# Optimization experiments

Measured on AMD Instinct MI355X. Metric: run time of the kernel, lower is better.

The kernel has to match this reference:

```python
import jax, jax.numpy as jnp
import numpy as np
from jax.scipy.special import logsumexp

B, D, A = 64, 128, 128


def setup_inputs() -> dict:
    key = jax.random.key(0)
    k1, k2, k3, k4 = jax.random.split(key, 4)
    x = jax.random.randint(k1, (B, D), 0, 2).astype(jnp.float32)  # binary observations
    u_log_p_a1 = jax.random.normal(k2, (1, 1, 1, A), dtype=jnp.float32)
    u_log_transition = jax.random.normal(k3, (D - 1, A, A), dtype=jnp.float32)
    log_p_xi_g_ai = jax.random.normal(k4, (1, D, 1, A), dtype=jnp.float32)
    return {
        "x": x,
        "u_log_p_a1": u_log_p_a1,
        "u_log_transition": u_log_transition,
        "log_p_xi_g_ai": log_p_xi_g_ai,
    }


def reference(x, u_log_p_a1, u_log_transition, log_p_xi_g_ai):
    b, d = x.shape
    a = u_log_p_a1.shape[-1]
    # _normalize_logits == log_softmax along last dim
    log_p_a1 = jax.nn.log_softmax(u_log_p_a1, axis=-1)          # [1,1,1,A]
    log_T = jax.nn.log_softmax(u_log_transition, axis=-1)        # [D-1,A,A]
    # Bernoulli(logits=l).log_prob(v) = v*l - softplus(l)
    l = log_p_xi_g_ai                                            # [1,D,1,A]
    log_px_vec = x[:, :, None, None] * l - jax.nn.softplus(l)    # [B,D,1,A]
    # per-step reduction matrices
    red = log_px_vec[:, 1:] + log_T                              # [B,D-1,A,A]
    # initial matrix: row-repeated initial vector
    init = jnp.broadcast_to(log_px_vec[:, 0] + log_p_a1[0], (b, a, a))  # [B,A,A]
    mats = jnp.transpose(red, (1, 0, 2, 3))                      # [D-1,B,A,A]

    def step(M, T):
        # log-space matmul: new[b,i,j] = logsumexp_k M[b,i,k] + T[b,k,j]
        new = logsumexp(M[:, :, :, None] + T[:, None, :, :], axis=2)
        return new, None

    final, _ = jax.lax.scan(step, init, mats)                    # [B,A,A]
    log_px = logsumexp(final, axis=-1)                           # [B,A] (rows identical)
    return (log_px, log_p_a1)
```

## Files before the change

### kernel.cpp

```cpp
#include <hip/hip_runtime.h>


#define B_ 64
#define D_ 128
#define A_ 128
#define T_ 127

#define E16_UINTS (T_ * 8192)
#define BC_OFF E16_UINTS
#define BC_SZ (B_ * T_ * A_)
#define LP_OFF (BC_OFF + BC_SZ)

typedef _Float16 h2 __attribute__((ext_vector_type(2)));

__device__ __forceinline__ float dot2acc(unsigned int e, unsigned int s, float acc) {
    return __builtin_amdgcn_fdot2(__builtin_bit_cast(h2, e),
                                  __builtin_bit_cast(h2, s), acc, false);
}
__device__ __forceinline__ int packrtz(float a, float b) {
    auto p = __builtin_amdgcn_cvt_pkrtz(a, b);
    return __builtin_bit_cast(int, p);
}

template <int CTRL>
__device__ __forceinline__ float dpp_mov_self(float x) {
    return __int_as_float(__builtin_amdgcn_update_dpp(
        __float_as_int(x), __float_as_int(x), CTRL, 0xF, 0xF, false));
}
template <int CTRL>
__device__ __forceinline__ float dpp_mov_zero(float x) {
    return __int_as_float(__builtin_amdgcn_update_dpp(
        0, __float_as_int(x), CTRL, 0xF, 0xF, true));
}
__device__ __forceinline__ float wave_max_partial(float x) {
    x = fmaxf(x, dpp_mov_self<0x111>(x));
    x = fmaxf(x, dpp_mov_self<0x112>(x));
    x = fmaxf(x, dpp_mov_self<0x114>(x));
    x = fmaxf(x, dpp_mov_self<0x118>(x));
    x = fmaxf(x, dpp_mov_self<0x142>(x));
    x = fmaxf(x, dpp_mov_self<0x143>(x));
    return x;
}
__device__ __forceinline__ float wave_max_bcast(float x) {
    return __int_as_float(__builtin_amdgcn_readlane(
        __float_as_int(wave_max_partial(x)), 63));
}
__device__ __forceinline__ float wave_sum_bcast(float x) {
    x += dpp_mov_zero<0x111>(x);
    x += dpp_mov_zero<0x112>(x);
    x += dpp_mov_zero<0x114>(x);
    x += dpp_mov_zero<0x118>(x);
    x += dpp_mov_zero<0x142>(x);
    x += dpp_mov_zero<0x143>(x);
    return __int_as_float(__builtin_amdgcn_readlane(__float_as_int(x), 63));
}

__global__ __launch_bounds__(256) void prep(const float* __restrict__ uT,
                                            const float* __restrict__ u1,
                                            const float* __restrict__ x,
                                            const float* __restrict__ lg,
                                            float* __restrict__ ws,
                                            float* __restrict__ out) {
    __shared__ float ul[128 * 128];
    const int t = blockIdx.x, tid = threadIdx.x;
    const float* u = uT + (size_t)t * A_ * A_;

    for (int i = tid; i < 4096; i += 256) {
        float4 v4 = ((const float4*)u)[i];
        *(float4*)&ul[(i >> 5) * 128 + (i & 31) * 4] = v4;
    }
    __syncthreads();

    if (tid < 128) {
        const int r = tid;
        float mx = -1e30f;
        for (int it = 0; it < 128; it++) mx = fmaxf(mx, ul[r * 128 + ((it + r) & 127)]);
        float s = 0.f;
        for (int it = 0; it < 128; it++) s += __expf(ul[r * 128 + ((it + r) & 127)] - mx);
        float Z = mx + __logf(s);
        for (int it = 0; it < 128; it++) ul[r * 128 + ((it + r) & 127)] -= Z;
    }
    __syncthreads();

    unsigned int* Et = (unsigned int*)ws + (size_t)t * 8192;
    for (int it = 0; it < 32; it++) {
        int a = it * 256 + tid;
        int c = a & 3, j = (a >> 2) & 127, q = a >> 9;
        int i = 4 * q + c;
        float e0 = __expf(ul[(2 * i) * 128 + j]);
        float e1 = __expf(ul[(2 * i + 1) * 128 + j]);
        Et[a] = (unsigned int)packrtz(e0, e1);
    }

    {
        int j = tid & 127, hb = tid >> 7;
        float lv = lg[(t + 1) * A_ + j];
        float sp = (lv > 0.f) ? (lv + log1pf(__expf(-lv))) : log1pf(__expf(lv));
        float g0 = -sp, g1 = lv - sp;
        float* BC = ws + BC_OFF;
        for (int b = hb * 32; b < hb * 32 + 32; b++) {
            float xv = x[b * D_ + t + 1];
            BC[((size_t)b * T_ + t) * A_ + j] = (xv != 0.f) ? g1 : g0;
        }
    }

    if (t == 0 && tid < 64) {
        int lane = tid;
        float a = u1[lane], c = u1[lane + 64];
        float mx = wave_max_bcast(fmaxf(a, c));
        float s = wave_sum_bcast(__expf(a - mx) + __expf(c - mx));
        float lse = mx + __logf(s);
        ws[LP_OFF + lane] = a - lse;
        ws[LP_OFF + lane + 64] = c - lse;
        out[B_ * A_ + lane] = a - lse;
        out[B_ * A_ + lane + 64] = c - lse;
    }
}

#define BARRIER() asm volatile("s_waitcnt lgkmcnt(0)\n\ts_barrier" ::: "memory")

#define STEP(T, EC, EP, BCC, BCP, DOPF)                                       \
    {                                                                         \
        const int p = (T) & 1, np = p ^ 1;                                    \
        if (DOPF) {                                    \
            const uint4* pfp = (const uint4*)(Eb + (size_t)((T) + 1) * 32768);\
            _Pragma("unroll") for (int q = 0; q < 16; q++) EP[q] = pfp[q*128];\
            BCP = BCg[((T) + 1) * A_];                                        \
            __builtin_amdgcn_sched_barrier(0);                                \
        }                                                                     \
        float2 vm2 = *(const float2*)&vml[p][0];                              \
        float Mcur = fmaxf(vm2.x, vm2.y);                                     \
        const uint4* ewp = (const uint4*)&ewl[p][0];                          \
        float a0 = 0, a1 = 0, a2 = 0, a3 = 0;                                 \
        _Pragma("unroll") for (int q = 0; q < 16; q++) {                      \
            uint4 e = ewp[q];                                                 \
            a0 = dot2acc(EC[q].x, e.x, a0);                                   \
            a1 = dot2acc(EC[q].y, e.y, a1);                                   \
            a2 = dot2acc(EC[q].z, e.z, a2);                                   \
            a3 = dot2acc(EC[q].w, e.w, a3);                                   \
        }                                                                     \
        float S = (a0 + a1) + (a2 + a3);                                      \
        float vnew = __logf(S) + Mp + BCC;                                    \
        ewl[np][j] = (_Float16)__expf(vnew - Mcur);   \
        float wm = wave_max_partial(vnew);             \
        if (lane == 63) vml[np][w] = wm;                                      \
        v = vnew;                                                             \
        Mp = Mcur;                                                            \
        BARRIER();                                                            \
    }

__global__ __launch_bounds__(128) void fwd(const float* __restrict__ x,
                                           const float* __restrict__ lg,
                                           const float* __restrict__ ws,
                                           float* __restrict__ out) {
    __shared__ __align__(16) _Float16 ewl[2][A_];
    __shared__ float vml[2][2];
    __shared__ float sums[2];
    const int b = blockIdx.x, tid = threadIdx.x;
    const int w = tid >> 6, lane = tid & 63;
    const int j = 64 * w + lane;

    const char* Eb = (const char*)ws + j * 16;
    const float* BCg = ws + BC_OFF + (size_t)b * T_ * A_ + j;
    const float* LP = ws + LP_OFF;

    float ll = lg[j];
    float sp = (ll > 0.f) ? (ll + log1pf(__expf(-ll))) : log1pf(__expf(ll));
    float xv0 = x[b * D_];
    float v = LP[j] + ((xv0 != 0.f) ? (ll - sp) : (-sp));
    float wm0 = wave_max_bcast(v);
    if (lane == 0) vml[0][w] = wm0;
    BARRIER();
    float Mp = fmaxf(vml[0][0], vml[0][1]);
    ewl[0][j] = (_Float16)__expf(v - Mp);

    uint4 E0[16], E1[16];
    float bc0, bc1;
    {
        const uint4* p0 = (const uint4*)(Eb);
#pragma unroll
        for (int q = 0; q < 16; q++) E0[q] = p0[q * 128];
        bc0 = BCg[0];
        __builtin_amdgcn_sched_barrier(0);
    }
    bc1 = 0.f;
    BARRIER();

    for (int t = 0; t < 126; t += 2) {
        STEP(t + 0, E0, E1, bc0, bc1, 1)
        STEP(t + 1, E1, E0, bc1, bc0, 1)
    }
    STEP(126, E0, E1, bc0, bc1, 0)

    float Mf = fmaxf(vml[1][0], vml[1][1]);
    float sw = wave_sum_bcast(__expf(v - Mf));
    if (lane == 0) sums[w] = sw;
    BARRIER();
    float L = Mf + __logf(sums[0] + sums[1]);
    out[b * A_ + j] = L;
}

extern "C" void kernel_launch(void* const* d_in, const int* in_sizes, int n_in,
                              void* d_out, int out_size, void* d_ws, size_t ws_size,
                              hipStream_t stream) {
    const float* x = (const float*)d_in[0];
    const float* u1 = (const float*)d_in[1];
    const float* uT = (const float*)d_in[2];
    const float* lg = (const float*)d_in[3];
    float* ws = (float*)d_ws;
    float* out = (float*)d_out;

    prep<<<dim3(T_), dim3(256), 0, stream>>>(uT, u1, x, lg, ws, out);
    fwd<<<dim3(B_), dim3(128), 0, stream>>>(x, lg, ws, out);
}
```

Measured before the change: 177.1 us.

## Store transition exponentials as fp8 and stream them via global-to-LDS triple buffering

Transition probability matrices are now precomputed as scaled fp8 (x256, with the scale compensated in the emission bias) instead of fp16. The forward kernel uses 256 threads that split the k-reduction in halves across lanes, and it triple-buffers the per-step matrix through LDS with async global_load_lds instead of register prefetch. The goal is to halve memory traffic per step and hide load latency behind compute. Using fp8 adds significant quantization error to the log-likelihood recurrence, and the extra per-step __syncthreads plus unpack conversions add overhead.

```diff
diff --git a/kernel.cpp b/kernel.cpp
--- a/kernel.cpp
+++ b/kernel.cpp
@@ -5,22 +5,65 @@
 #define D_ 128
 #define A_ 128
 #define T_ 127
-
-#define E16_UINTS (T_ * 8192)
-#define BC_OFF E16_UINTS
+#define LN256 5.545177444479562f
+
+#define E8_UINTS (T_ * 4096)
+#define BC_OFF E8_UINTS
 #define BC_SZ (B_ * T_ * A_)
 #define LP_OFF (BC_OFF + BC_SZ)
 
-typedef _Float16 h2 __attribute__((ext_vector_type(2)));
-
-__device__ __forceinline__ float dot2acc(unsigned int e, unsigned int s, float acc) {
-    return __builtin_amdgcn_fdot2(__builtin_bit_cast(h2, e),
-                                  __builtin_bit_cast(h2, s), acc, false);
-}
-__device__ __forceinline__ int packrtz(float a, float b) {
-    auto p = __builtin_amdgcn_cvt_pkrtz(a, b);
-    return __builtin_bit_cast(int, p);
-}
+#define AS1C(p) ((const __attribute__((address_space(1))) void*)(p))
+#define AS3P(p) ((__attribute__((address_space(3))) void*)(p))
+
+typedef float f2v __attribute__((ext_vector_type(2)));
+
+#if __has_builtin(__builtin_amdgcn_cvt_pk_f32_fp8)
+template <int WORD>
+__device__ __forceinline__ f2v unpk(unsigned int u) {
+    return __builtin_amdgcn_cvt_pk_f32_fp8((int)u, WORD);
+}
+#else
+__device__ __forceinline__ float fp8b_to_f32(unsigned int b) {
+    unsigned int e = (b >> 3) & 15, m = b & 7;
+    if (e) return __uint_as_float(((e + 120) << 23) | (m << 20));
+    return (float)m * 0x1p-9f;
+}
+template <int WORD>
+__device__ __forceinline__ f2v unpk(unsigned int u) {
+    unsigned int b0 = (u >> (WORD ? 16 : 0)) & 255;
+    unsigned int b1 = (u >> (WORD ? 24 : 8)) & 255;
+    f2v r; r.x = fp8b_to_f32(b0); r.y = fp8b_to_f32(b1);
+    return r;
+}
+#endif
+
+#if __has_builtin(__builtin_amdgcn_cvt_pk_fp8_f32)
+__device__ __forceinline__ unsigned int pk4_fp8(float a, float b, float c, float d) {
+    int v = __builtin_amdgcn_cvt_pk_fp8_f32(a, b, 0, false);
+    v = __builtin_amdgcn_cvt_pk_fp8_f32(c, d, v, true);
+    return (unsigned int)v;
+}
+#else
+__device__ __forceinline__ unsigned int f32_to_fp8b(float f) {
+    if (f < 0.015625f) {
+        int m = (int)rintf(f * 512.f);
+        return (unsigned int)m;
+    }
+    unsigned int fb = __float_as_uint(f);
+    int ex = (int)((fb >> 23) & 255) - 127;
+    unsigned int mant = (fb >> 20) & 7;
+    unsigned int rem = fb & 0xFFFFFu;
+    if (rem > 0x80000u || (rem == 0x80000u && (mant & 1))) mant++;
+    int e8 = ex + 7;
+    if (mant == 8) { mant = 0; e8++; }
+    if (e8 > 15) return 0x7Eu;
+    return ((unsigned int)e8 << 3) | mant;
+}
+__device__ __forceinline__ unsigned int pk4_fp8(float a, float b, float c, float d) {
+    return f32_to_fp8b(a) | (f32_to_fp8b(b) << 8) |
+           (f32_to_fp8b(c) << 16) | (f32_to_fp8b(d) << 24);
+}
+#endif
 
 template <int CTRL>
 __device__ __forceinline__ float dpp_mov_self(float x) {
@@ -82,21 +125,26 @@
     }
     __syncthreads();
 
-    unsigned int* Et = (unsigned int*)ws + (size_t)t * 8192;
-    for (int it = 0; it < 32; it++) {
-        int a = it * 256 + tid;
-        int c = a & 3, j = (a >> 2) & 127, q = a >> 9;
-        int i = 4 * q + c;
-        float e0 = __expf(ul[(2 * i) * 128 + j]);
-        float e1 = __expf(ul[(2 * i + 1) * 128 + j]);
-        Et[a] = (unsigned int)packrtz(e0, e1);
+    unsigned int* Et = (unsigned int*)ws + (size_t)t * 4096;
+    for (int it = 0; it < 16; it++) {
+        int m = it * 256 + tid;
+        int g = m >> 7;
+        int c = g >> 3, h = (g >> 2) & 1, w = g & 3;
+        int jl = (m >> 2) & 31;
+        int k0 = 64 * h + 16 * c + 4 * (m & 3);
+        int j = 32 * w + jl;
+        float f0 = 256.f * __expf(ul[(k0 + 0) * 128 + j]);
+        float f1 = 256.f * __expf(ul[(k0 + 1) * 128 + j]);
+        float f2 = 256.f * __expf(ul[(k0 + 2) * 128 + j]);
+        float f3 = 256.f * __expf(ul[(k0 + 3) * 128 + j]);
+        Et[m] = pk4_fp8(f0, f1, f2, f3);
     }
 
     {
         int j = tid & 127, hb = tid >> 7;
         float lv = lg[(t + 1) * A_ + j];
         float sp = (lv > 0.f) ? (lv + log1pf(__expf(-lv))) : log1pf(__expf(lv));
-        float g0 = -sp, g1 = lv - sp;
+        float g0 = -sp - LN256, g1 = lv - sp - LN256;
         float* BC = ws + BC_OFF;
         for (int b = hb * 32; b < hb * 32 + 32; b++) {
             float xv = x[b * D_ + t + 1];
@@ -117,87 +165,116 @@
     }
 }
 
-#define BARRIER() asm volatile("s_waitcnt lgkmcnt(0)\n\ts_barrier" ::: "memory")
-
-#define STEP(T, EC, EP, BCC, BCP, DOPF)                                       \
+#define STEP(T, BUFC, BUFN, P, DOISSUE)                                       \
     {                                                                         \
-        const int p = (T) & 1, np = p ^ 1;                                    \
-        if (DOPF) {                                    \
-            const uint4* pfp = (const uint4*)(Eb + (size_t)((T) + 1) * 32768);\
-            _Pragma("unroll") for (int q = 0; q < 16; q++) EP[q] = pfp[q*128];\
-            BCP = BCg[((T) + 1) * A_];                                        \
-            __builtin_amdgcn_sched_barrier(0);                                \
+        __syncthreads();                                                      \
+        uint4 ec0 = *(const uint4*)&Ebuf[BUFC][((0 + h) * 4 + w) * 512 + jl * 16]; \
+        uint4 ec1 = *(const uint4*)&Ebuf[BUFC][((2 + h) * 4 + w) * 512 + jl * 16]; \
+        uint4 ec2 = *(const uint4*)&Ebuf[BUFC][((4 + h) * 4 + w) * 512 + jl * 16]; \
+        uint4 ec3 = *(const uint4*)&Ebuf[BUFC][((6 + h) * 4 + w) * 512 + jl * 16]; \
+        if (DOISSUE) {                                                        \
+            _Pragma("unroll") for (int i = 0; i < 4; i++)                     \
+                __builtin_amdgcn_global_load_lds(                             \
+                    AS1C(Eg + ((size_t)(T) + 2) * 16384 + (w * 4 + i) * 1024  \
+                         + lane * 16),                                        \
+                    AS3P(&Ebuf[BUFN][(w * 4 + i) * 1024]), 16, 0, 0);         \
         }                                                                     \
-        float2 vm2 = *(const float2*)&vml[p][0];                              \
-        float Mcur = fmaxf(vm2.x, vm2.y);                                     \
-        const uint4* ewp = (const uint4*)&ewl[p][0];                          \
+        float4 vm = *(const float4*)&vml[P][0];                               \
+        float Mv = fmaxf(fmaxf(vm.x, vm.y), fmaxf(vm.z, vm.w));               \
         float a0 = 0, a1 = 0, a2 = 0, a3 = 0;                                 \
-        _Pragma("unroll") for (int q = 0; q < 16; q++) {                      \
-            uint4 e = ewp[q];                                                 \
-            a0 = dot2acc(EC[q].x, e.x, a0);                                   \
-            a1 = dot2acc(EC[q].y, e.y, a1);                                   \
-            a2 = dot2acc(EC[q].z, e.z, a2);                                   \
-            a3 = dot2acc(EC[q].w, e.w, a3);                                   \
+        _Pragma("unroll") for (int c = 0; c < 4; c++) {                       \
+            uint4 ec = (c == 0) ? ec0 : (c == 1) ? ec1 : (c == 2) ? ec2 : ec3;\
+            const float4* ewp = (const float4*)&ewf[P][64 * h + 16 * c];      \
+            float4 w0 = ewp[0], w1 = ewp[1], w2 = ewp[2], w3 = ewp[3];        \
+            f2v p0 = unpk<0>(ec.x), p1 = unpk<1>(ec.x);                       \
+            a0 += p0.x * w0.x; a1 += p0.y * w0.y;                             \
+            a2 += p1.x * w0.z; a3 += p1.y * w0.w;                             \
+            f2v p2 = unpk<0>(ec.y), p3 = unpk<1>(ec.y);                       \
+            a0 += p2.x * w1.x; a1 += p2.y * w1.y;                             \
+            a2 += p3.x * w1.z; a3 += p3.y * w1.w;                             \
+            f2v p4 = unpk<0>(ec.z), p5 = unpk<1>(ec.z);                       \
+            a0 += p4.x * w2.x; a1 += p4.y * w2.y;                             \
+            a2 += p5.x * w2.z; a3 += p5.y * w2.w;                             \
+            f2v p6 = unpk<0>(ec.w), p7 = unpk<1>(ec.w);                       \
+            a0 += p6.x * w3.x; a1 += p6.y * w3.y;                             \
+            a2 += p7.x * w3.z; a3 += p7.y * w3.w;                             \
         }                                                                     \
         float S = (a0 + a1) + (a2 + a3);                                      \
-        float vnew = __logf(S) + Mp + BCC;                                    \
-        ewl[np][j] = (_Float16)__expf(vnew - Mcur);   \
-        float wm = wave_max_partial(vnew);             \
-        if (lane == 63) vml[np][w] = wm;                                      \
+        S += __shfl_xor(S, 32, 64);                                           \
+        float vnew = __logf(S) + Mn + bcc;                                    \
+        if (h == 0) ewf[P ^ 1][j] = __expf(vnew - Mv);                        \
+        float wmx = wave_max_partial(vnew);                                   \
+        if (lane == 63) vml[P ^ 1][w] = wmx;                                  \
         v = vnew;                                                             \
-        Mp = Mcur;                                                            \
-        BARRIER();                                                            \
-    }
-
-__global__ __launch_bounds__(128) void fwd(const float* __restrict__ x,
-                                           const float* __restrict__ lg,
-                                           const float* __restrict__ ws,
-                                           float* __restrict__ out) {
-    __shared__ __align__(16) _Float16 ewl[2][A_];
-    __shared__ float vml[2][2];
-    __shared__ float sums[2];
+        Mn = Mv;                                                              \
+        bcc = bcn;                                                            \
+        if (DOISSUE) bcn = BCg[((T) + 2) * A_];                               \
+    }
+
+__global__ __launch_bounds__(256, 1) void fwd(const float* __restrict__ x,
+                                              const float* __restrict__ lg,
+                                              const float* __restrict__ ws,
+                                              float* __restrict__ out) {
+    __shared__ __align__(16) char Ebuf[3][16384];
+    __shared__ __align__(16) float ewf[2][A_];
+    __shared__ __align__(16) float vml[2][4];
+    __shared__ float sums[4];
     const int b = blockIdx.x, tid = threadIdx.x;
     const int w = tid >> 6, lane = tid & 63;
-    const int j = 64 * w + lane;
-
-    const char* Eb = (const char*)ws + j * 16;
+    const int h = lane >> 5, jl = lane & 31;
+    const int j = 32 * w + jl;
+
+    const char* Eg = (const char*)ws;
     const float* BCg = ws + BC_OFF + (size_t)b * T_ * A_ + j;
     const float* LP = ws + LP_OFF;
+
+#pragma unroll
+    for (int i = 0; i < 4; i++) {
+        __builtin_amdgcn_global_load_lds(
+            AS1C(Eg + (w * 4 + i) * 1024 + lane * 16),
+            AS3P(&Ebuf[0][(w * 4 + i) * 1024]), 16, 0, 0);
+        __builtin_amdgcn_global_load_lds(
+            AS1C(Eg + 16384 + (w * 4 + i) * 1024 + lane * 16),
+            AS3P(&Ebuf[1][(w * 4 + i) * 1024]), 16, 0, 0);
+    }
+    float bcc = BCg[0];
+    float bcn = BCg[A_];
 
     float ll = lg[j];
     float sp = (ll > 0.f) ? (ll + log1pf(__expf(-ll))) : log1pf(__expf(ll));
     float xv0 = x[b * D_];
     float v = LP[j] + ((xv0 != 0.f) ? (ll - sp) : (-sp));
-    float wm0 = wave_max_bcast(v);
-    if (lane == 0) vml[0][w] = wm0;
-    BARRIER();
-    float Mp = fmaxf(vml[0][0], vml[0][1]);
-    ewl[0][j] = (_Float16)__expf(v - Mp);
-
-    uint4 E0[16], E1[16];
-    float bc0, bc1;
-    {
-        const uint4* p0 = (const uint4*)(Eb);
-#pragma unroll
-        for (int q = 0; q < 16; q++) E0[q] = p0[q * 128];
-        bc0 = BCg[0];
-        __builtin_amdgcn_sched_barrier(0);
-    }
-    bc1 = 0.f;
-    BARRIER();
-
-    for (int t = 0; t < 126; t += 2) {
-        STEP(t + 0, E0, E1, bc0, bc1, 1)
-        STEP(t + 1, E1, E0, bc1, bc0, 1)
-    }
-    STEP(126, E0, E1, bc0, bc1, 0)
-
-    float Mf = fmaxf(vml[1][0], vml[1][1]);
-    float sw = wave_sum_bcast(__expf(v - Mf));
+    float wm0 = wave_max_partial(v);
+    if (lane == 63) vml[0][w] = wm0;
+    __syncthreads();
+    float4 vm0 = *(const float4*)&vml[0][0];
+    float Mn = fmaxf(fmaxf(vm0.x, vm0.y), fmaxf(vm0.z, vm0.w));
+    if (h == 0) ewf[0][j] = __expf(v - Mn);
+
+    for (int t = 0; t < 120; t += 6) {
+        STEP(t + 0, 0, 2, 0, 1)
+        STEP(t + 1, 1, 0, 1, 1)
+        STEP(t + 2, 2, 1, 0, 1)
+        STEP(t + 3, 0, 2, 1, 1)
+        STEP(t + 4, 1, 0, 0, 1)
+        STEP(t + 5, 2, 1, 1, 1)
+    }
+    STEP(120, 0, 2, 0, 1)
+    STEP(121, 1, 0, 1, 1)
+    STEP(122, 2, 1, 0, 1)
+    STEP(123, 0, 2, 1, 1)
+    STEP(124, 1, 0, 0, 1)
+    STEP(125, 2, 1, 1, 0)
+    STEP(126, 0, 2, 0, 0)
+
+    __syncthreads();
+    float4 vmf = *(const float4*)&vml[1][0];
+    float Mf = fmaxf(fmaxf(vmf.x, vmf.y), fmaxf(vmf.z, vmf.w));
+    float sw = wave_sum_bcast(__expf(v - Mf)) * 0.5f;
     if (lane == 0) sums[w] = sw;
-    BARRIER();
-    float L = Mf + __logf(sums[0] + sums[1]);
-    out[b * A_ + j] = L;
+    __syncthreads();
+    float L = Mf + __logf((sums[0] + sums[1]) + (sums[2] + sums[3]));
+    if (tid < A_) out[b * A_ + tid] = L;
 }
 
 extern "C" void kernel_launch(void* const* d_in, const int* in_sizes, int n_in,
@@ -211,5 +288,5 @@
     float* out = (float*)d_out;
 
     prep<<<dim3(T_), dim3(256), 0, stream>>>(uT, u1, x, lg, ws, out);
-    fwd<<<dim3(B_), dim3(128), 0, stream>>>(x, lg, ws, out);
-}
+    fwd<<<dim3(B_), dim3(256), 0, stream>>>(x, lg, ws, out);
+}
```

After: 212.9 us. 20.3% more time.

## Move forward recursion to linear-domain scaling and split the K reduction across half-waves

Applied to the files above, without the earlier changes.

The emission term is now precomputed in exp space, so each step multiplies by it instead of taking a log and exp per element. The running max is handled as a multiplicative rescale whose log is accumulated in beta. The fwd kernel doubles to 256 threads, and each output column's 128-wide dot product is split across two half-waves and combined with a shuffle. Prefetch of the next step's transition tiles uses hand-written global loads with explicit vmcnt waits, and the workspace E layout is permuted to match. This shortens the per-step serial chain of transcendentals and halves the register footprint for E. The cost is an extra shuffle and risk of fp16 range issues in the linear domain.

```diff
diff --git a/kernel.cpp b/kernel.cpp
--- a/kernel.cpp
+++ b/kernel.cpp
@@ -7,19 +7,20 @@
 #define T_ 127
 
 #define E16_UINTS (T_ * 8192)
-#define BC_OFF E16_UINTS
-#define BC_SZ (B_ * T_ * A_)
-#define LP_OFF (BC_OFF + BC_SZ)
+#define G_OFF E16_UINTS
+#define G_SZ (B_ * T_ * A_)
+#define LP_OFF (G_OFF + G_SZ)
 
 typedef _Float16 h2 __attribute__((ext_vector_type(2)));
-
+typedef unsigned int u32x4 __attribute__((ext_vector_type(4)));
+
+__device__ __forceinline__ int packrtz(float a, float b) {
+    auto p = __builtin_amdgcn_cvt_pkrtz(a, b);
+    return __builtin_bit_cast(int, p);
+}
 __device__ __forceinline__ float dot2acc(unsigned int e, unsigned int s, float acc) {
     return __builtin_amdgcn_fdot2(__builtin_bit_cast(h2, e),
                                   __builtin_bit_cast(h2, s), acc, false);
-}
-__device__ __forceinline__ int packrtz(float a, float b) {
-    auto p = __builtin_amdgcn_cvt_pkrtz(a, b);
-    return __builtin_bit_cast(int, p);
 }
 
 template <int CTRL>
@@ -85,8 +86,10 @@
     unsigned int* Et = (unsigned int*)ws + (size_t)t * 8192;
     for (int it = 0; it < 32; it++) {
         int a = it * 256 + tid;
-        int c = a & 3, j = (a >> 2) & 127, q = a >> 9;
-        int i = 4 * q + c;
+        int c = a & 3, jl = (a >> 2) & 31, w = (a >> 7) & 3;
+        int h = (a >> 9) & 1, q = a >> 10;
+        int i = 32 * h + 4 * q + c;
+        int j = 32 * w + jl;
         float e0 = __expf(ul[(2 * i) * 128 + j]);
         float e1 = __expf(ul[(2 * i + 1) * 128 + j]);
         Et[a] = (unsigned int)packrtz(e0, e1);
@@ -96,11 +99,11 @@
         int j = tid & 127, hb = tid >> 7;
         float lv = lg[(t + 1) * A_ + j];
         float sp = (lv > 0.f) ? (lv + log1pf(__expf(-lv))) : log1pf(__expf(lv));
-        float g0 = -sp, g1 = lv - sp;
-        float* BC = ws + BC_OFF;
+        float G0 = __expf(-sp), G1 = __expf(lv - sp);
+        float* G = ws + G_OFF;
         for (int b = hb * 32; b < hb * 32 + 32; b++) {
             float xv = x[b * D_ + t + 1];
-            BC[((size_t)b * T_ + t) * A_ + j] = (xv != 0.f) ? g1 : g0;
+            G[((size_t)b * T_ + t) * A_ + j] = (xv != 0.f) ? G1 : G0;
         }
     }
 
@@ -119,85 +122,114 @@
 
 #define BARRIER() asm volatile("s_waitcnt lgkmcnt(0)\n\ts_barrier" ::: "memory")
 
-#define STEP(T, EC, EP, BCC, BCP, DOPF)                                       \
+#define ISSUE(EN, GN, TT)                                                     \
+    {                                                                         \
+        unsigned long long ab = Ebase + (unsigned long long)(TT) * 32768ull;  \
+        _Pragma("unroll") for (int q = 0; q < 8; q++)                         \
+            asm volatile("global_load_dwordx4 %0, %1, off"                    \
+                         : "=v"(EN[q])                                        \
+                         : "v"(ab + (unsigned long long)(q * 4096)));         \
+        asm volatile("global_load_dword %0, %1, off"                          \
+                     : "=v"(GN)                                               \
+                     : "v"(Gbase + (unsigned long long)(TT) * 512ull));       \
+    }
+
+#define WAITON(EC, GC, CNT)                                                   \
+    asm volatile("s_waitcnt vmcnt(" #CNT ")"                                  \
+                 : "+v"(EC[0]), "+v"(EC[1]), "+v"(EC[2]), "+v"(EC[3]),        \
+                   "+v"(EC[4]), "+v"(EC[5]), "+v"(EC[6]), "+v"(EC[7]),        \
+                   "+v"(GC));
+
+#define BODY(T, EC, GC)                                                       \
     {                                                                         \
         const int p = (T) & 1, np = p ^ 1;                                    \
-        if (DOPF) {                                    \
-            const uint4* pfp = (const uint4*)(Eb + (size_t)((T) + 1) * 32768);\
-            _Pragma("unroll") for (int q = 0; q < 16; q++) EP[q] = pfp[q*128];\
-            BCP = BCg[((T) + 1) * A_];                                        \
-            __builtin_amdgcn_sched_barrier(0);                                \
-        }                                                                     \
-        float2 vm2 = *(const float2*)&vml[p][0];                              \
-        float Mcur = fmaxf(vm2.x, vm2.y);                                     \
-        const uint4* ewp = (const uint4*)&ewl[p][0];                          \
+        float4 vm4 = *(const float4*)&vml[p][0];                              \
+        float maxW = fmaxf(fmaxf(vm4.x, vm4.y), fmaxf(vm4.z, vm4.w));         \
+        float srec = 1.0f / maxW;                                             \
+        beta += __logf(mprev);               \
+        mprev = maxW;                                                         \
+        const uint4* ewp = (const uint4*)&ewl[p][0] + h * 8;                  \
         float a0 = 0, a1 = 0, a2 = 0, a3 = 0;                                 \
-        _Pragma("unroll") for (int q = 0; q < 16; q++) {                      \
-            uint4 e = ewp[q];                                                 \
-            a0 = dot2acc(EC[q].x, e.x, a0);                                   \
-            a1 = dot2acc(EC[q].y, e.y, a1);                                   \
-            a2 = dot2acc(EC[q].z, e.z, a2);                                   \
-            a3 = dot2acc(EC[q].w, e.w, a3);                                   \
+        _Pragma("unroll") for (int q = 0; q < 8; q++) {                       \
+            uint4 ew4 = ewp[q];                                               \
+            a0 = dot2acc(EC[q].x, ew4.x, a0);                                 \
+            a1 = dot2acc(EC[q].y, ew4.y, a1);                                 \
+            a2 = dot2acc(EC[q].z, ew4.z, a2);                                 \
+            a3 = dot2acc(EC[q].w, ew4.w, a3);                                 \
         }                                                                     \
         float S = (a0 + a1) + (a2 + a3);                                      \
-        float vnew = __logf(S) + Mp + BCC;                                    \
-        ewl[np][j] = (_Float16)__expf(vnew - Mcur);   \
-        float wm = wave_max_partial(vnew);             \
-        if (lane == 63) vml[np][w] = wm;                                      \
-        v = vnew;                                                             \
-        Mp = Mcur;                                                            \
+        S += __shfl_xor(S, 32, 64);                                           \
+        float W = S * GC;                                                     \
+        if (h == 0) ewl[np][j] = (_Float16)(W * srec);                        \
+        float wm = wave_max_partial(W);                         \
+        if (lane == 63) vml[np][wv] = wm;                                     \
+        Wlast = W;                                                            \
         BARRIER();                                                            \
     }
 
-__global__ __launch_bounds__(128) void fwd(const float* __restrict__ x,
-                                           const float* __restrict__ lg,
-                                           const float* __restrict__ ws,
-                                           float* __restrict__ out) {
+#define STEPP(T, EC, EN, GC, GN)                                              \
+    {                                                                         \
+        ISSUE(EN, GN, (T) + 1)                                                \
+        WAITON(EC, GC, 9)                                                     \
+        BODY(T, EC, GC)                                                       \
+    }
+#define STEPL(T, EC, GC)                                                      \
+    {                                                                         \
+        WAITON(EC, GC, 0)                                                     \
+        BODY(T, EC, GC)                                                       \
+    }
+
+__global__ __launch_bounds__(256, 1) void fwd(const float* __restrict__ x,
+                                              const float* __restrict__ lg,
+                                              const float* __restrict__ ws,
+                                              float* __restrict__ out) {
     __shared__ __align__(16) _Float16 ewl[2][A_];
-    __shared__ float vml[2][2];
-    __shared__ float sums[2];
+    __shared__ __align__(16) float vml[2][4];
+    __shared__ float sums[4];
     const int b = blockIdx.x, tid = threadIdx.x;
-    const int w = tid >> 6, lane = tid & 63;
-    const int j = 64 * w + lane;
-
-    const char* Eb = (const char*)ws + j * 16;
-    const float* BCg = ws + BC_OFF + (size_t)b * T_ * A_ + j;
+    const int wv = tid >> 6, lane = tid & 63;
+    const int h = lane >> 5, jl = lane & 31;
+    const int j = 32 * wv + jl;
+
+    const unsigned long long Ebase =
+        (unsigned long long)ws + (unsigned long long)(h * 2048 + wv * 512 + jl * 16);
+    const unsigned long long Gbase =
+        (unsigned long long)(ws + G_OFF + (size_t)b * T_ * A_ + j);
     const float* LP = ws + LP_OFF;
+
+    u32x4 EA[8], EB[8];
+    float gA, gB;
+    ISSUE(EA, gA, 0)
 
     float ll = lg[j];
     float sp = (ll > 0.f) ? (ll + log1pf(__expf(-ll))) : log1pf(__expf(ll));
     float xv0 = x[b * D_];
-    float v = LP[j] + ((xv0 != 0.f) ? (ll - sp) : (-sp));
-    float wm0 = wave_max_bcast(v);
-    if (lane == 0) vml[0][w] = wm0;
+    float v0 = LP[j] + ((xv0 != 0.f) ? (ll - sp) : (-sp));
+    float wm0 = wave_max_partial(v0);
+    if (lane == 63) vml[0][wv] = wm0;
     BARRIER();
-    float Mp = fmaxf(vml[0][0], vml[0][1]);
-    ewl[0][j] = (_Float16)__expf(v - Mp);
-
-    uint4 E0[16], E1[16];
-    float bc0, bc1;
-    {
-        const uint4* p0 = (const uint4*)(Eb);
-#pragma unroll
-        for (int q = 0; q < 16; q++) E0[q] = p0[q * 128];
-        bc0 = BCg[0];
-        __builtin_amdgcn_sched_barrier(0);
-    }
-    bc1 = 0.f;
+    float4 vmi = *(const float4*)&vml[0][0];
+    float M0 = fmaxf(fmaxf(vmi.x, vmi.y), fmaxf(vmi.z, vmi.w));
+    float w0 = __expf(v0 - M0);
+    if (h == 0) ewl[0][j] = (_Float16)w0;
+    float wmW = wave_max_partial(w0);
+    if (lane == 63) vml[0][wv] = wmW;
     BARRIER();
 
+    float beta = M0, mprev = 1.0f, Wlast = 0.f;
+
     for (int t = 0; t < 126; t += 2) {
-        STEP(t + 0, E0, E1, bc0, bc1, 1)
-        STEP(t + 1, E1, E0, bc1, bc0, 1)
-    }
-    STEP(126, E0, E1, bc0, bc1, 0)
-
-    float Mf = fmaxf(vml[1][0], vml[1][1]);
-    float sw = wave_sum_bcast(__expf(v - Mf));
-    if (lane == 0) sums[w] = sw;
-    BARRIER();
-    float L = Mf + __logf(sums[0] + sums[1]);
-    out[b * A_ + j] = L;
+        STEPP(t + 0, EA, EB, gA, gB)
+        STEPP(t + 1, EB, EA, gB, gA)
+    }
+    STEPL(126, EA, gA)
+
+    float sw = wave_sum_bcast(Wlast) * 0.5f;
+    if (lane == 0) sums[wv] = sw;
+    __syncthreads();
+    float tot = (sums[0] + sums[1]) + (sums[2] + sums[3]);
+    float L = beta + __logf(tot);
+    if (tid < A_) out[b * A_ + tid] = L;
 }
 
 extern "C" void kernel_launch(void* const* d_in, const int* in_sizes, int n_in,
@@ -211,5 +243,5 @@
     float* out = (float*)d_out;
 
     prep<<<dim3(T_), dim3(256), 0, stream>>>(uT, u1, x, lg, ws, out);
-    fwd<<<dim3(B_), dim3(128), 0, stream>>>(x, lg, ws, out);
-}
+    fwd<<<dim3(B_), dim3(256), 0, stream>>>(x, lg, ws, out);
+}
```

After: 169.1 us. 4.5% less time.
